# Kernel optimization log

Measured on AMD Instinct MI355X. Metric: run time of the kernel, lower is better.

The kernel has to match this reference:

```python
import jax, jax.numpy as jnp
import numpy as np

N_NODES = 50000
N_EDGES = 800000
IN_CH = 256
OUT_CH = 128
HID = 2 * OUT_CH  # 256
N_GRAPHS = 64


def setup_inputs() -> dict:
    key = jax.random.key(0)
    k = jax.random.split(key, 8)
    x = jax.random.normal(k[0], (N_NODES, IN_CH), dtype=jnp.float32)
    edge_index = jax.random.randint(k[1], (2, N_EDGES), 0, N_NODES, dtype=jnp.int64)
    batch = jnp.sort(jax.random.randint(k[2], (N_NODES,), 0, N_GRAPHS, dtype=jnp.int64))
    # GCNConv parameters (glorot-ish init)
    W1 = jax.random.normal(k[3], (IN_CH, HID), dtype=jnp.float32) / np.sqrt(IN_CH)
    b1 = jnp.zeros((HID,), dtype=jnp.float32)
    W2 = jax.random.normal(k[4], (HID, OUT_CH), dtype=jnp.float32) / np.sqrt(HID)
    b2 = jnp.zeros((OUT_CH,), dtype=jnp.float32)
    return {"x": x, "W1": W1, "b1": b1, "W2": W2, "b2": b2,
            "edge_index": edge_index, "batch": batch}


def _gcn_conv(x, W, b, src, dst, n):
    """PyG GCNConv: transform, then sym-normalized aggregation with self-loops."""
    h = x @ W  # [N, F_out]
    # degree over destination nodes, including the added self-loop
    deg = jnp.zeros((n,), dtype=h.dtype).at[dst].add(1.0) + 1.0
    dinv = jax.lax.rsqrt(deg)
    norm = dinv[src] * dinv[dst]            # [E]
    agg = jnp.zeros_like(h).at[dst].add(h[src] * norm[:, None])
    agg = agg + h * (1.0 / deg)[:, None]    # self-loop contribution: deg_i^{-1}
    return agg + b


def reference(x, W1, b1, W2, b2, edge_index, batch):
    src, dst = edge_index[0], edge_index[1]
    # dropout is identity in eval mode (training=False)
    h = jax.nn.elu(_gcn_conv(x, W1, b1, src, dst, N_NODES))
    h = _gcn_conv(h, W2, b2, src, dst, N_NODES)
    # global mean pool over graphs
    ones = jnp.ones((N_NODES,), dtype=h.dtype)
    counts = jax.ops.segment_sum(ones, batch, num_segments=N_GRAPHS)
    sums = jax.ops.segment_sum(h, batch, num_segments=N_GRAPHS)
    return sums / jnp.maximum(counts, 1.0)[:, None]
```

## Files before the change

kernel.cpp:

```cpp
#include <hip/hip_runtime.h>
#include <hip/hip_bf16.h>

#define N_NODES 50000
#define N_EDGES 800000
#define IN_CH 256
#define HID 256
#define OUT_CH 128
#define N_GRAPHS 64
#define SCAN_BLOCKS 196
#define M_PAD 50048
#define COUNT_BLOCKS 3125
#define CVTX_BLOCKS  12512
#define CVTW_BLOCKS  384
#define GEMM1_BLOCKS 782
#define SROW 50048
#define S_QUARTER 12512
#define GEMM2_BLOCKS 391
#define SBUILD_BLOCKS 256
#define T2_BLOCKS 391
#define T2_KC 128
#define RED_BLOCKS 128

typedef __bf16 bf16x8 __attribute__((ext_vector_type(8)));
typedef float f32x4 __attribute__((ext_vector_type(4)));
typedef unsigned short u16x8 __attribute__((ext_vector_type(8)));

__device__ __forceinline__ float bf2f(unsigned short u) {
    union { unsigned int i; float f; } x; x.i = ((unsigned int)u) << 16; return x.f;
}
__device__ __forceinline__ unsigned short f2bf(float f) {
    union { float f; unsigned int i; } x; x.f = f;
    unsigned int r = x.i + 0x7FFFu + ((x.i >> 16) & 1u);
    return (unsigned short)(r >> 16);
}

__device__ __forceinline__ float lo_f(unsigned int u) {
    return __uint_as_float(u << 16);
}
__device__ __forceinline__ float hi_f(unsigned int u) {
    return __uint_as_float(u & 0xFFFF0000u);
}

__device__ __forceinline__ void load16(const void* g, void* l) {
    __builtin_amdgcn_global_load_lds(
        (const __attribute__((address_space(1))) void*)g,
        (__attribute__((address_space(3))) void*)l, 16, 0, 0);
}

__device__ __forceinline__ int rp(const int* __restrict__ rl,
                                  const int* __restrict__ boff, int i) {
    return rl[i] + boff[i >> 8];
}

__global__ __launch_bounds__(256) void count_cvtx_cvtw_kernel(
        const int* __restrict__ ei, int* __restrict__ cnt, int* __restrict__ erank,
        const float* __restrict__ x, unsigned short* __restrict__ xb,
        const float* __restrict__ W1, const float* __restrict__ W2,
        unsigned short* __restrict__ w1t, unsigned short* __restrict__ w2t) {
    int b = blockIdx.x;
    if (b < COUNT_BLOCKS) {
        int e = b * 256 + threadIdx.x;
        erank[e] = atomicAdd(&cnt[ei[N_EDGES + e]], 1);
        return;
    }
    b -= COUNT_BLOCKS;
    if (b < CVTX_BLOCKS) {
        int i = b * 256 + threadIdx.x;
        ushort4 o;
        if (i < N_NODES * (IN_CH / 4)) {
            float4 v = ((const float4*)x)[i];
            o.x = f2bf(v.x); o.y = f2bf(v.y); o.z = f2bf(v.z); o.w = f2bf(v.w);
        } else {
            o = make_ushort4(0, 0, 0, 0);
        }
        ((ushort4*)xb)[i] = o;
        return;
    }
    int i = (b - CVTX_BLOCKS) * 256 + threadIdx.x;
    if (i < HID * IN_CH) {
        int n = i >> 8, k = i & 255;
        w1t[i] = f2bf(W1[k * HID + n]);
    } else {
        int j = i - HID * IN_CH;
        int n = j >> 8, k = j & 255;
        w2t[j] = f2bf(W2[k * OUT_CH + n]);
    }
}

__global__ __launch_bounds__(256) void scan_a_kernel(const int* __restrict__ cnt,
                                                     int* __restrict__ rl,
                                                     int* __restrict__ blocksum,
                                                     float* __restrict__ dinv,
                                                     float* __restrict__ invdeg,
                                                     const int* __restrict__ batch,
                                                     int* __restrict__ rstart) {
    __shared__ int tmp[256];
    int t = threadIdx.x;
    int i = blockIdx.x * 256 + t;
    int v = (i < N_NODES) ? cnt[i] : 0;
    int x = v;
    tmp[t] = x;
    __syncthreads();
    if (i < N_NODES) {
        int bg = batch[i];
        int bp = (i > 0) ? batch[i - 1] : -1;
        for (int g = bp + 1; g <= bg; g++) rstart[g] = i;
        if (i == N_NODES - 1)
            for (int g = bg + 1; g <= N_GRAPHS; g++) rstart[g] = N_NODES;
    }
#pragma unroll
    for (int off = 1; off < 256; off <<= 1) {
        int y = (t >= off) ? tmp[t - off] : 0;
        __syncthreads();
        x += y;
        tmp[t] = x;
        __syncthreads();
    }
    if (i <= N_NODES) rl[i] = x - v;
    if (i < N_NODES) {
        float d = (float)v + 1.0f;
        dinv[i] = rsqrtf(d);
        invdeg[i] = 1.0f / d;
    }
    if (t == 255) blocksum[blockIdx.x] = x;
}

__global__ __launch_bounds__(256) void scanb1_kernel(const int* __restrict__ blocksum,
                                                     int* __restrict__ blockoff) {
    __shared__ int tmp[256];
    int t = threadIdx.x;
    int v = (t < SCAN_BLOCKS) ? blocksum[t] : 0;
    int x = v;
    tmp[t] = x;
    __syncthreads();
#pragma unroll
    for (int off = 1; off < 256; off <<= 1) {
        int y = (t >= off) ? tmp[t - off] : 0;
        __syncthreads();
        x += y;
        tmp[t] = x;
        __syncthreads();
    }
    if (t < SCAN_BLOCKS) blockoff[t] = x - v;
}

template <int TR>
__device__ __forceinline__ void gemm_body(const unsigned short* __restrict__ A,
                                          const unsigned short* __restrict__ Bt,
                                          unsigned short* __restrict__ C,
                                          int N, int bxx, int byy, char* As, char* Bs) {
    const int K = 256;
    int tid = threadIdx.x;
    int bm = bxx * 128;
    int bn = byy * 128;
    int lane = tid & 63, wave = tid >> 6;
    int lane15 = lane & 15, quad = lane >> 4;
    int wm0 = (wave >> 1) << 6;
    int wn0 = (wave & 1) << 6;

    int s1 = tid, s2 = tid + 256;
    int r1 = s1 >> 2, q1 = (s1 & 3) ^ ((r1 >> 1) & 3);
    int r2 = s2 >> 2, q2 = (s2 & 3) ^ ((r2 >> 1) & 3);
    const char* gA1 = (const char*)(A + (size_t)(bm + r1) * K) + (q1 << 4);
    const char* gA2 = (const char*)(A + (size_t)(bm + r2) * K) + (q2 << 4);
    const char* gB1 = (const char*)(Bt + (size_t)(bn + r1) * K) + (q1 << 4);
    const char* gB2 = (const char*)(Bt + (size_t)(bn + r2) * K) + (q2 << 4);
    char* lA1 = As + (wave << 10);
    char* lA2 = As + 4096 + (wave << 10);
    char* lB1 = Bs + (wave << 10);
    char* lB2 = Bs + 4096 + (wave << 10);

    int swm = (lane15 >> 1) & 3;
    f32x4 acc[4][4];
#pragma unroll
    for (int mt = 0; mt < 4; mt++)
#pragma unroll
        for (int nt = 0; nt < 4; nt++)
            acc[mt][nt] = (f32x4){0.f, 0.f, 0.f, 0.f};

    for (int k0 = 0; k0 < K; k0 += 32) {
        __syncthreads();
        load16(gA1 + (k0 << 1), lA1);
        load16(gA2 + (k0 << 1), lA2);
        load16(gB1 + (k0 << 1), lB1);
        load16(gB2 + (k0 << 1), lB2);
        __syncthreads();
        bf16x8 af[4], bfr[4];
#pragma unroll
        for (int t = 0; t < 4; t++) {
            int ra = wm0 + t * 16 + lane15;
            af[t] = *(const bf16x8*)(As + ra * 64 + ((quad ^ swm) << 4));
            int rb = wn0 + t * 16 + lane15;
            bfr[t] = *(const bf16x8*)(Bs + rb * 64 + ((quad ^ swm) << 4));
        }
#pragma unroll
        for (int mt = 0; mt < 4; mt++)
#pragma unroll
            for (int nt = 0; nt < 4; nt++)
                acc[mt][nt] = __builtin_amdgcn_mfma_f32_16x16x32_bf16(
                    af[mt], bfr[nt], acc[mt][nt], 0, 0, 0);
    }

#pragma unroll
    for (int mt = 0; mt < 4; mt++) {
        int rowb = bm + wm0 + mt * 16 + quad * 4;
#pragma unroll
        for (int nt = 0; nt < 4; nt++) {
            int col = bn + wn0 + nt * 16 + lane15;
            f32x4 a = acc[mt][nt];
            if (TR == 0) {
                C[(size_t)(rowb + 0) * N + col] = f2bf(a[0]);
                C[(size_t)(rowb + 1) * N + col] = f2bf(a[1]);
                C[(size_t)(rowb + 2) * N + col] = f2bf(a[2]);
                C[(size_t)(rowb + 3) * N + col] = f2bf(a[3]);
            } else {
                ushort4 o;
                o.x = f2bf(a[0]); o.y = f2bf(a[1]);
                o.z = f2bf(a[2]); o.w = f2bf(a[3]);
                *(ushort4*)(C + (size_t)col * M_PAD + rowb) = o;
            }
        }
    }
}

__global__ __launch_bounds__(256) void fill_gemm1_kernel(
        const int* __restrict__ ei,
        const int* __restrict__ rl,
        const int* __restrict__ boff,
        const int* __restrict__ erank,
        int2* __restrict__ edge2,
        const float* __restrict__ dinv,
        const unsigned short* __restrict__ xb,
        const unsigned short* __restrict__ w1t,
        unsigned short* __restrict__ h1b) {
    __shared__ char As[8192];
    __shared__ char Bs[8192];
    int b = blockIdx.x;
    if (b < GEMM1_BLOCKS) {
        gemm_body<0>(xb, w1t, h1b, HID, b % 391, b / 391, As, Bs);
        return;
    }
    int e = (b - GEMM1_BLOCKS) * 256 + threadIdx.x;
    if (e >= N_EDGES) return;
    int s = ei[e];
    int d = ei[N_EDGES + e];
    int p = rp(rl, boff, d) + erank[e];
    float w = dinv[s] * dinv[d];
    edge2[p] = make_int2(s, __float_as_int(w));
}

__global__ __launch_bounds__(256) void agg1_kernel(const unsigned short* __restrict__ h,
                                                   const float* __restrict__ bias,
                                                   const int* __restrict__ rl,
                                                   const int* __restrict__ boff,
                                                   const int2* __restrict__ edge2,
                                                   const float* __restrict__ invdeg,
                                                   unsigned short* __restrict__ out) {
    int node = blockIdx.x * 4 + (threadIdx.x >> 6);
    int lane = threadIdx.x & 63;
    if (node >= N_NODES) {
        if (node < M_PAD)
            ((ushort4*)out)[(size_t)node * 64 + lane] = make_ushort4(0, 0, 0, 0);
        return;
    }
    const uint2* h4 = (const uint2*)h;
    float id = invdeg[node];
    uint2 sv = h4[(size_t)node * 64 + lane];
    f32x4 acc = (f32x4){lo_f(sv.x) * id, hi_f(sv.x) * id,
                        lo_f(sv.y) * id, hi_f(sv.y) * id};
    int e0 = rp(rl, boff, node);
    int e1 = rp(rl, boff, node + 1);
    int e = e0;
    for (; e + 15 < e1; e += 16) {
        int2 ed[16];
        uint2 v[16];
#pragma unroll
        for (int j = 0; j < 16; j++) ed[j] = edge2[e + j];
#pragma unroll
        for (int j = 0; j < 16; j++) v[j] = h4[(size_t)ed[j].x * 64 + lane];
#pragma unroll
        for (int j = 0; j < 16; j++) {
            float w = __int_as_float(ed[j].y);
            f32x4 vf = (f32x4){lo_f(v[j].x), hi_f(v[j].x),
                               lo_f(v[j].y), hi_f(v[j].y)};
            acc += vf * w;
        }
    }
    for (; e + 7 < e1; e += 8) {
        int2 ed[8];
        uint2 v[8];
#pragma unroll
        for (int j = 0; j < 8; j++) ed[j] = edge2[e + j];
#pragma unroll
        for (int j = 0; j < 8; j++) v[j] = h4[(size_t)ed[j].x * 64 + lane];
#pragma unroll
        for (int j = 0; j < 8; j++) {
            float w = __int_as_float(ed[j].y);
            f32x4 vf = (f32x4){lo_f(v[j].x), hi_f(v[j].x),
                               lo_f(v[j].y), hi_f(v[j].y)};
            acc += vf * w;
        }
    }
    for (; e + 3 < e1; e += 4) {
        int2 ed[4];
        uint2 v[4];
#pragma unroll
        for (int j = 0; j < 4; j++) ed[j] = edge2[e + j];
#pragma unroll
        for (int j = 0; j < 4; j++) v[j] = h4[(size_t)ed[j].x * 64 + lane];
#pragma unroll
        for (int j = 0; j < 4; j++) {
            float w = __int_as_float(ed[j].y);
            f32x4 vf = (f32x4){lo_f(v[j].x), hi_f(v[j].x),
                               lo_f(v[j].y), hi_f(v[j].y)};
            acc += vf * w;
        }
    }
    for (; e < e1; e++) {
        int2 ed0 = edge2[e];
        float w0 = __int_as_float(ed0.y);
        uint2 v0 = h4[(size_t)ed0.x * 64 + lane];
        f32x4 vf = (f32x4){lo_f(v0.x), hi_f(v0.x), lo_f(v0.y), hi_f(v0.y)};
        acc += vf * w0;
    }
    float4 bb = ((const float4*)bias)[lane];
    acc[0] += bb.x; acc[1] += bb.y; acc[2] += bb.z; acc[3] += bb.w;
    acc[0] = acc[0] > 0.f ? acc[0] : expm1f(acc[0]);
    acc[1] = acc[1] > 0.f ? acc[1] : expm1f(acc[1]);
    acc[2] = acc[2] > 0.f ? acc[2] : expm1f(acc[2]);
    acc[3] = acc[3] > 0.f ? acc[3] : expm1f(acc[3]);
    ushort4 o;
    o.x = f2bf(acc[0]); o.y = f2bf(acc[1]); o.z = f2bf(acc[2]); o.w = f2bf(acc[3]);
    ((ushort4*)out)[(size_t)node * 64 + lane] = o;
}

__global__ __launch_bounds__(256) void gemm2_sbuild_kernel(
        const unsigned short* __restrict__ A,
        const unsigned short* __restrict__ Bt,
        unsigned short* __restrict__ C,
        const int2* __restrict__ edge2,
        const int* __restrict__ rl,
        const int* __restrict__ boff,
        const int* __restrict__ rstart,
        const float* __restrict__ invdeg,
        float* __restrict__ Sp) {
    __shared__ float srow[S_QUARTER];
    int b = blockIdx.x;
    if (b < GEMM2_BLOCKS) {
        gemm_body<1>(A, Bt, C, OUT_CH, b, 0, (char*)srow, (char*)srow + 8192);
        return;
    }
    int sb = b - GEMM2_BLOCKS;
    int g = sb >> 2;
    int base = (sb & 3) * S_QUARTER;
    int t = threadIdx.x;
    for (int i = t; i < S_QUARTER; i += 256) srow[i] = 0.f;
    int n0 = rstart[g], n1 = rstart[g + 1];
    __syncthreads();
    int e0 = rp(rl, boff, n0);
    int e1 = rp(rl, boff, n1);
    for (int e = e0 + t; e < e1; e += 256) {
        int2 ed = edge2[e];
        unsigned int s = (unsigned int)(ed.x - base);
        if (s < S_QUARTER)
            atomicAdd(&srow[s], __int_as_float(ed.y));
    }
    __syncthreads();
    float ic = 1.0f / fmaxf((float)(n1 - n0), 1.0f);
    float* Sg = Sp + (size_t)g * SROW + base;
    for (int i = t; i < S_QUARTER; i += 256) {
        float v = srow[i];
        int col = base + i;
        if (col >= n0 && col < n1) v += invdeg[col];
        Sg[i] = v * ic;
    }
}

__global__ __launch_bounds__(256) void t2_kernel(const float* __restrict__ Sp,
                                                 const unsigned short* __restrict__ h2t,
                                                 float* __restrict__ part) {
    int b = blockIdx.x;
    int k0 = b * T2_KC;
    int tid = threadIdx.x;
    int lane = tid & 63, wave = tid >> 6;
    int lane15 = lane & 15, quad = lane >> 4;
    int cb = wave << 5;
    f32x4 acc[4][2];
#pragma unroll
    for (int m = 0; m < 4; m++) {
        acc[m][0] = (f32x4){0.f, 0.f, 0.f, 0.f};
        acc[m][1] = (f32x4){0.f, 0.f, 0.f, 0.f};
    }
    const unsigned short* hr0 = h2t + (size_t)(cb + lane15) * M_PAD;
    const unsigned short* hr1 = h2t + (size_t)(cb + 16 + lane15) * M_PAD;
#pragma unroll
    for (int ks = 0; ks < T2_KC / 32; ks++) {
        int k = k0 + ks * 32 + quad * 8;
        bf16x8 b0 = *(const bf16x8*)(hr0 + k);
        bf16x8 b1 = *(const bf16x8*)(hr1 + k);
#pragma unroll
        for (int m = 0; m < 4; m++) {
            const float* ap = Sp + (size_t)(m * 16 + lane15) * SROW + k;
            f32x4 v0 = *(const f32x4*)ap;
            f32x4 v1 = *(const f32x4*)(ap + 4);
            u16x8 hu, lu;
#pragma unroll
            for (int j = 0; j < 4; j++) {
                unsigned int e0 = __float_as_uint(v0[j]);
                hu[j] = (unsigned short)(e0 >> 16);
                lu[j] = f2bf(v0[j] - __uint_as_float(e0 & 0xFFFF0000u));
                unsigned int e1 = __float_as_uint(v1[j]);
                hu[j + 4] = (unsigned short)(e1 >> 16);
                lu[j + 4] = f2bf(v1[j] - __uint_as_float(e1 & 0xFFFF0000u));
            }
            bf16x8 ah = __builtin_bit_cast(bf16x8, hu);
            bf16x8 al = __builtin_bit_cast(bf16x8, lu);
            acc[m][0] = __builtin_amdgcn_mfma_f32_16x16x32_bf16(ah, b0, acc[m][0], 0, 0, 0);
            acc[m][0] = __builtin_amdgcn_mfma_f32_16x16x32_bf16(al, b0, acc[m][0], 0, 0, 0);
            acc[m][1] = __builtin_amdgcn_mfma_f32_16x16x32_bf16(ah, b1, acc[m][1], 0, 0, 0);
            acc[m][1] = __builtin_amdgcn_mfma_f32_16x16x32_bf16(al, b1, acc[m][1], 0, 0, 0);
        }
    }
    float* pb = part + (size_t)b * (N_GRAPHS * OUT_CH);
#pragma unroll
    for (int m = 0; m < 4; m++) {
        int g0 = m * 16 + quad * 4;
#pragma unroll
        for (int nt = 0; nt < 2; nt++) {
            int c = cb + nt * 16 + lane15;
            f32x4 a = acc[m][nt];
#pragma unroll
            for (int j = 0; j < 4; j++)
                pb[(g0 + j) * OUT_CH + c] = a[j];
        }
    }
}

__global__ __launch_bounds__(256) void t2red_kernel(const float* __restrict__ part,
                                                    const float* __restrict__ b2,
                                                    const int* __restrict__ rstart,
                                                    float* __restrict__ out) {
    __shared__ float red[4][64];
    int tid = threadIdx.x;
    int q = tid >> 6, l = tid & 63;
    int o = blockIdx.x * 64 + l;
    float s = 0.f;
    for (int i = q; i < T2_BLOCKS; i += 4)
        s += part[(size_t)i * (N_GRAPHS * OUT_CH) + o];
    red[q][l] = s;
    __syncthreads();
    if (tid < 64) {
        float tot = red[0][l] + red[1][l] + red[2][l] + red[3][l];
        int g = o >> 7, c = o & 127;
        out[o] = (rstart[g + 1] > rstart[g]) ? tot + b2[c] : 0.f;
    }
}

extern "C" void kernel_launch(void* const* d_in, const int* in_sizes, int n_in,
                              void* d_out, int out_size, void* d_ws, size_t ws_size,
                              hipStream_t stream) {
    const float* x  = (const float*)d_in[0];
    const float* W1 = (const float*)d_in[1];
    const float* b1 = (const float*)d_in[2];
    const float* W2 = (const float*)d_in[3];
    const float* b2 = (const float*)d_in[4];
    const int*   ei = (const int*)d_in[5];
    const int*   batch = (const int*)d_in[6];
    float* out = (float*)d_out;

    unsigned short* xb  = (unsigned short*)d_ws;
    unsigned short* h1b = xb  + (size_t)M_PAD * IN_CH;
    unsigned short* hBb = h1b + (size_t)M_PAD * HID;
    unsigned short* h2t = hBb + (size_t)M_PAD * HID;
    unsigned short* w1t = h2t + (size_t)OUT_CH * M_PAD;
    unsigned short* w2t = w1t + HID * IN_CH;
    float* dinv   = (float*)(w2t + OUT_CH * HID);
    float* invdeg = dinv + N_NODES;
    int*   rl     = (int*)(invdeg + N_NODES);
    int2*  edge2  = (int2*)(rl + 50016);
    int*   cnt    = (int*)(edge2 + N_EDGES);
    int*   erank  = cnt + N_NODES;
    int*   blocksum = erank + N_EDGES;
    int*   blockoff = blocksum + 256;
    int*   rstart   = blockoff + 256;
    float* Sp     = (float*)(rstart + 80);
    float* part   = (float*)xb;

    hipMemsetAsync(cnt, 0, (size_t)N_NODES * 4, stream);

    count_cvtx_cvtw_kernel<<<COUNT_BLOCKS + CVTX_BLOCKS + CVTW_BLOCKS, 256, 0, stream>>>(
        ei, cnt, erank, x, xb, W1, W2, w1t, w2t);
    scan_a_kernel<<<SCAN_BLOCKS, 256, 0, stream>>>(cnt, rl, blocksum, dinv, invdeg,
                                                   batch, rstart);
    scanb1_kernel<<<1, 256, 0, stream>>>(blocksum, blockoff);
    fill_gemm1_kernel<<<GEMM1_BLOCKS + COUNT_BLOCKS, 256, 0, stream>>>(
        ei, rl, blockoff, erank, edge2, dinv, xb, w1t, h1b);
    agg1_kernel<<<M_PAD / 4, 256, 0, stream>>>(h1b, b1, rl, blockoff,
                                               edge2, invdeg, hBb);
    gemm2_sbuild_kernel<<<GEMM2_BLOCKS + SBUILD_BLOCKS, 256, 0, stream>>>(
        hBb, w2t, h2t, edge2, rl, blockoff, rstart, invdeg, Sp);
    t2_kernel<<<T2_BLOCKS, 256, 0, stream>>>(Sp, h2t, part);
    t2red_kernel<<<RED_BLOCKS, 256, 0, stream>>>(part, b2, rstart, out);
}
```

Measured before the change: 300.6 us.

## Split degree counters 8-way, fuse block-offset scan via decoupled lookback, drop edge weights

```diff
diff --git a/kernel.cpp b/kernel.cpp
--- a/kernel.cpp
+++ b/kernel.cpp
@@ -20,6 +20,7 @@
 #define T2_BLOCKS 391
 #define T2_KC 128
 #define RED_BLOCKS 128
+#define CNT8_STRIDE 50016
 
 typedef __bf16 bf16x8 __attribute__((ext_vector_type(8)));
 typedef float f32x4 __attribute__((ext_vector_type(4)));
@@ -47,20 +48,16 @@
         (__attribute__((address_space(3))) void*)l, 16, 0, 0);
 }
 
-__device__ __forceinline__ int rp(const int* __restrict__ rl,
-                                  const int* __restrict__ boff, int i) {
-    return rl[i] + boff[i >> 8];
-}
-
 __global__ __launch_bounds__(256) void count_cvtx_cvtw_kernel(
-        const int* __restrict__ ei, int* __restrict__ cnt, int* __restrict__ erank,
+        const int* __restrict__ ei, int* __restrict__ cnt8, int* __restrict__ erank,
         const float* __restrict__ x, unsigned short* __restrict__ xb,
         const float* __restrict__ W1, const float* __restrict__ W2,
         unsigned short* __restrict__ w1t, unsigned short* __restrict__ w2t) {
     int b = blockIdx.x;
     if (b < COUNT_BLOCKS) {
         int e = b * 256 + threadIdx.x;
-        erank[e] = atomicAdd(&cnt[ei[N_EDGES + e]], 1);
+        int d = ei[N_EDGES + e];
+        erank[e] = atomicAdd(&cnt8[(b & 7) * CNT8_STRIDE + d], 1);
         return;
     }
     b -= COUNT_BLOCKS;
@@ -87,17 +84,28 @@
     }
 }
 
-__global__ __launch_bounds__(256) void scan_a_kernel(const int* __restrict__ cnt,
+__global__ __launch_bounds__(256) void scan_a_kernel(const int* __restrict__ cnt8,
                                                      int* __restrict__ rl,
-                                                     int* __restrict__ blocksum,
                                                      float* __restrict__ dinv,
                                                      float* __restrict__ invdeg,
                                                      const int* __restrict__ batch,
-                                                     int* __restrict__ rstart) {
+                                                     int* __restrict__ rstart,
+                                                     int* __restrict__ offs8,
+                                                     unsigned int* __restrict__ scanflag) {
     __shared__ int tmp[256];
     int t = threadIdx.x;
     int i = blockIdx.x * 256 + t;
-    int v = (i < N_NODES) ? cnt[i] : 0;
+    int v = 0;
+    if (i < N_NODES) {
+        int off = 0;
+#pragma unroll
+        for (int k = 0; k < 8; k++) {
+            int c = cnt8[k * CNT8_STRIDE + i];
+            offs8[k * CNT8_STRIDE + i] = off;
+            off += c;
+        }
+        v = off;
+    }
     int x = v;
     tmp[t] = x;
     __syncthreads();
@@ -116,32 +124,33 @@
         tmp[t] = x;
         __syncthreads();
     }
-    if (i <= N_NODES) rl[i] = x - v;
+    if (t == 255)
+        __hip_atomic_store(&scanflag[blockIdx.x], (unsigned int)x | 0x80000000u,
+                           __ATOMIC_RELEASE, __HIP_MEMORY_SCOPE_AGENT);
+    unsigned int part = 0;
+    if (t < blockIdx.x) {
+        unsigned int f;
+        do {
+            f = __hip_atomic_load(&scanflag[t], __ATOMIC_ACQUIRE,
+                                  __HIP_MEMORY_SCOPE_AGENT);
+        } while (!(f & 0x80000000u));
+        part = f & 0x7FFFFFFFu;
+    }
+    __syncthreads();
+    tmp[t] = (int)part;
+    __syncthreads();
+#pragma unroll
+    for (int off = 128; off >= 1; off >>= 1) {
+        if (t < off) tmp[t] += tmp[t + off];
+        __syncthreads();
+    }
+    int boffv = tmp[0];
+    if (i <= N_NODES) rl[i] = boffv + x - v;
     if (i < N_NODES) {
         float d = (float)v + 1.0f;
         dinv[i] = rsqrtf(d);
         invdeg[i] = 1.0f / d;
     }
-    if (t == 255) blocksum[blockIdx.x] = x;
-}
-
-__global__ __launch_bounds__(256) void scanb1_kernel(const int* __restrict__ blocksum,
-                                                     int* __restrict__ blockoff) {
-    __shared__ int tmp[256];
-    int t = threadIdx.x;
-    int v = (t < SCAN_BLOCKS) ? blocksum[t] : 0;
-    int x = v;
-    tmp[t] = x;
-    __syncthreads();
-#pragma unroll
-    for (int off = 1; off < 256; off <<= 1) {
-        int y = (t >= off) ? tmp[t - off] : 0;
-        __syncthreads();
-        x += y;
-        tmp[t] = x;
-        __syncthreads();
-    }
-    if (t < SCAN_BLOCKS) blockoff[t] = x - v;
 }
 
 template <int TR>
@@ -226,10 +235,9 @@
 __global__ __launch_bounds__(256) void fill_gemm1_kernel(
         const int* __restrict__ ei,
         const int* __restrict__ rl,
-        const int* __restrict__ boff,
+        const int* __restrict__ offs8,
         const int* __restrict__ erank,
-        int2* __restrict__ edge2,
-        const float* __restrict__ dinv,
+        int* __restrict__ esrc,
         const unsigned short* __restrict__ xb,
         const unsigned short* __restrict__ w1t,
         unsigned short* __restrict__ h1b) {
@@ -244,16 +252,16 @@
     if (e >= N_EDGES) return;
     int s = ei[e];
     int d = ei[N_EDGES + e];
-    int p = rp(rl, boff, d) + erank[e];
-    float w = dinv[s] * dinv[d];
-    edge2[p] = make_int2(s, __float_as_int(w));
+    int k = (e >> 8) & 7;
+    int p = rl[d] + offs8[k * CNT8_STRIDE + d] + erank[e];
+    esrc[p] = s;
 }
 
 __global__ __launch_bounds__(256) void agg1_kernel(const unsigned short* __restrict__ h,
                                                    const float* __restrict__ bias,
                                                    const int* __restrict__ rl,
-                                                   const int* __restrict__ boff,
-                                                   const int2* __restrict__ edge2,
+                                                   const int* __restrict__ esrc,
+                                                   const float* __restrict__ dinv,
                                                    const float* __restrict__ invdeg,
                                                    unsigned short* __restrict__ out) {
     int node = blockIdx.x * 4 + (threadIdx.x >> 6);
@@ -265,61 +273,68 @@
     }
     const uint2* h4 = (const uint2*)h;
     float id = invdeg[node];
+    float dvd = dinv[node];
     uint2 sv = h4[(size_t)node * 64 + lane];
     f32x4 acc = (f32x4){lo_f(sv.x) * id, hi_f(sv.x) * id,
                         lo_f(sv.y) * id, hi_f(sv.y) * id};
-    int e0 = rp(rl, boff, node);
-    int e1 = rp(rl, boff, node + 1);
+    int e0 = rl[node];
+    int e1 = rl[node + 1];
     int e = e0;
     for (; e + 15 < e1; e += 16) {
-        int2 ed[16];
+        int sj[16];
         uint2 v[16];
-#pragma unroll
-        for (int j = 0; j < 16; j++) ed[j] = edge2[e + j];
-#pragma unroll
-        for (int j = 0; j < 16; j++) v[j] = h4[(size_t)ed[j].x * 64 + lane];
+        float ws[16];
+#pragma unroll
+        for (int j = 0; j < 16; j++) sj[j] = esrc[e + j];
+#pragma unroll
+        for (int j = 0; j < 16; j++) v[j] = h4[(size_t)sj[j] * 64 + lane];
+#pragma unroll
+        for (int j = 0; j < 16; j++) ws[j] = dinv[sj[j]] * dvd;
 #pragma unroll
         for (int j = 0; j < 16; j++) {
-            float w = __int_as_float(ed[j].y);
             f32x4 vf = (f32x4){lo_f(v[j].x), hi_f(v[j].x),
                                lo_f(v[j].y), hi_f(v[j].y)};
-            acc += vf * w;
+            acc += vf * ws[j];
         }
     }
     for (; e + 7 < e1; e += 8) {
-        int2 ed[8];
+        int sj[8];
         uint2 v[8];
-#pragma unroll
-        for (int j = 0; j < 8; j++) ed[j] = edge2[e + j];
-#pragma unroll
-        for (int j = 0; j < 8; j++) v[j] = h4[(size_t)ed[j].x * 64 + lane];
+        float ws[8];
+#pragma unroll
+        for (int j = 0; j < 8; j++) sj[j] = esrc[e + j];
+#pragma unroll
+        for (int j = 0; j < 8; j++) v[j] = h4[(size_t)sj[j] * 64 + lane];
+#pragma unroll
+        for (int j = 0; j < 8; j++) ws[j] = dinv[sj[j]] * dvd;
 #pragma unroll
         for (int j = 0; j < 8; j++) {
-            float w = __int_as_float(ed[j].y);
             f32x4 vf = (f32x4){lo_f(v[j].x), hi_f(v[j].x),
                                lo_f(v[j].y), hi_f(v[j].y)};
-            acc += vf * w;
+            acc += vf * ws[j];
         }
     }
     for (; e + 3 < e1; e += 4) {
-        int2 ed[4];
+        int sj[4];
         uint2 v[4];
-#pragma unroll
-        for (int j = 0; j < 4; j++) ed[j] = edge2[e + j];
-#pragma unroll
-        for (int j = 0; j < 4; j++) v[j] = h4[(size_t)ed[j].x * 64 + lane];
+        float ws[4];
+#pragma unroll
+        for (int j = 0; j < 4; j++) sj[j] = esrc[e + j];
+#pragma unroll
+        for (int j = 0; j < 4; j++) v[j] = h4[(size_t)sj[j] * 64 + lane];
+#pragma unroll
+        for (int j = 0; j < 4; j++) ws[j] = dinv[sj[j]] * dvd;
 #pragma unroll
         for (int j = 0; j < 4; j++) {
-            float w = __int_as_float(ed[j].y);
             f32x4 vf = (f32x4){lo_f(v[j].x), hi_f(v[j].x),
                                lo_f(v[j].y), hi_f(v[j].y)};
-            acc += vf * w;
+            acc += vf * ws[j];
         }
     }
     for (; e < e1; e++) {
-        int2 ed0 = edge2[e];
-        float w0 = __int_as_float(ed0.y);
-        uint2 v0 = h4[(size_t)ed0.x * 64 + lane];
+        int s0 = esrc[e];
+        float w0 = dinv[s0] * dvd;
+        uint2 v0 = h4[(size_t)s0 * 64 + lane];
         f32x4 vf = (f32x4){lo_f(v0.x), hi_f(v0.x), lo_f(v0.y), hi_f(v0.y)};
         acc += vf * w0;
     }
@@ -338,10 +353,10 @@
         const unsigned short* __restrict__ A,
         const unsigned short* __restrict__ Bt,
         unsigned short* __restrict__ C,
-        const int2* __restrict__ edge2,
+        const int* __restrict__ esrc,
         const int* __restrict__ rl,
-        const int* __restrict__ boff,
         const int* __restrict__ rstart,
+        const float* __restrict__ dinv,
         const float* __restrict__ invdeg,
         float* __restrict__ Sp) {
     __shared__ float srow[S_QUARTER];
@@ -357,13 +372,15 @@
     for (int i = t; i < S_QUARTER; i += 256) srow[i] = 0.f;
     int n0 = rstart[g], n1 = rstart[g + 1];
     __syncthreads();
-    int e0 = rp(rl, boff, n0);
-    int e1 = rp(rl, boff, n1);
-    for (int e = e0 + t; e < e1; e += 256) {
-        int2 ed = edge2[e];
-        unsigned int s = (unsigned int)(ed.x - base);
-        if (s < S_QUARTER)
-            atomicAdd(&srow[s], __int_as_float(ed.y));
+    for (int d = n0 + t; d < n1; d += 256) {
+        float dvd = dinv[d];
+        int ee1 = rl[d + 1];
+        for (int e = rl[d]; e < ee1; e++) {
+            int s = esrc[e];
+            unsigned int idx = (unsigned int)(s - base);
+            if (idx < S_QUARTER)
+                atomicAdd(&srow[idx], dinv[s] * dvd);
+        }
     }
     __syncthreads();
     float ic = 1.0f / fmaxf((float)(n1 - n0), 1.0f);
@@ -477,28 +494,26 @@
     float* dinv   = (float*)(w2t + OUT_CH * HID);
     float* invdeg = dinv + N_NODES;
     int*   rl     = (int*)(invdeg + N_NODES);
-    int2*  edge2  = (int2*)(rl + 50016);
-    int*   cnt    = (int*)(edge2 + N_EDGES);
-    int*   erank  = cnt + N_NODES;
-    int*   blocksum = erank + N_EDGES;
-    int*   blockoff = blocksum + 256;
-    int*   rstart   = blockoff + 256;
+    int*   esrc   = rl + 50016;
+    int*   cnt8   = esrc + N_EDGES;
+    unsigned int* scanflag = (unsigned int*)(cnt8 + 8 * CNT8_STRIDE);
+    int*   erank  = (int*)(scanflag + 256);
+    int*   offs8  = erank + N_EDGES;
+    int*   rstart = offs8 + 8 * CNT8_STRIDE;
     float* Sp     = (float*)(rstart + 80);
     float* part   = (float*)xb;
 
-    hipMemsetAsync(cnt, 0, (size_t)N_NODES * 4, stream);
+    hipMemsetAsync(cnt8, 0, (size_t)(8 * CNT8_STRIDE + 256) * 4, stream);
 
     count_cvtx_cvtw_kernel<<<COUNT_BLOCKS + CVTX_BLOCKS + CVTW_BLOCKS, 256, 0, stream>>>(
-        ei, cnt, erank, x, xb, W1, W2, w1t, w2t);
-    scan_a_kernel<<<SCAN_BLOCKS, 256, 0, stream>>>(cnt, rl, blocksum, dinv, invdeg,
-                                                   batch, rstart);
-    scanb1_kernel<<<1, 256, 0, stream>>>(blocksum, blockoff);
+        ei, cnt8, erank, x, xb, W1, W2, w1t, w2t);
+    scan_a_kernel<<<SCAN_BLOCKS, 256, 0, stream>>>(cnt8, rl, dinv, invdeg,
+                                                   batch, rstart, offs8, scanflag);
     fill_gemm1_kernel<<<GEMM1_BLOCKS + COUNT_BLOCKS, 256, 0, stream>>>(
-        ei, rl, blockoff, erank, edge2, dinv, xb, w1t, h1b);
-    agg1_kernel<<<M_PAD / 4, 256, 0, stream>>>(h1b, b1, rl, blockoff,
-                                               edge2, invdeg, hBb);
+        ei, rl, offs8, erank, esrc, xb, w1t, h1b);
+    agg1_kernel<<<M_PAD / 4, 256, 0, stream>>>(h1b, b1, rl, esrc, dinv, invdeg, hBb);
     gemm2_sbuild_kernel<<<GEMM2_BLOCKS + SBUILD_BLOCKS, 256, 0, stream>>>(
-        hBb, w2t, h2t, edge2, rl, blockoff, rstart, invdeg, Sp);
+        hBb, w2t, h2t, esrc, rl, rstart, dinv, invdeg, Sp);
     t2_kernel<<<T2_BLOCKS, 256, 0, stream>>>(Sp, h2t, part);
     t2red_kernel<<<RED_BLOCKS, 256, 0, stream>>>(part, b2, rstart, out);
 }
```

After: 337.1 us. 1.12x slower.
